# Optimization experiments

Hardware: AMD Instinct MI355X
Metric: run time of the kernel (lower is better)

Reference implementation:

```python
import jax, jax.numpy as jnp
import numpy as np

ALPHA = 1.8   # Levy stability index (undefined global in source; chosen heavy-tailed)
BETA = 0.0    # symmetric
SIGMA = 0.5
DEPTH = 25
DIM = 64
HID = 100
BATCH = 262144


def _levy_noise(u_raw, w_raw):
    """Chambers-Mallows-Stuck sampler for symmetric alpha-stable (beta=0).
    u_raw, w_raw ~ U(0,1); returns clipped noise, scale=0.1, clamp [-10,10]."""
    U = jnp.pi * (u_raw - 0.5)                       # U(-pi/2, pi/2)
    W = -jnp.log(jnp.clip(w_raw, 1e-12, 1.0))        # Exp(1)
    inv_a = 1.0 / ALPHA
    X = (jnp.sin(ALPHA * U) / jnp.cos(U) ** inv_a) * \
        (jnp.cos(U - ALPHA * U) / jnp.clip(W, 1e-12, None)) ** ((1.0 - ALPHA) * inv_a)
    return jnp.clip(0.1 * X, -10.0, 10.0)


def setup_inputs() -> dict:
    key = jax.random.key(0)
    ks = jax.random.split(key, 8)
    d, h = DIM, HID
    return {
        "x": jax.random.normal(ks[0], (BATCH, d), dtype=jnp.float32),
        "u_raw": jax.random.uniform(ks[1], (DEPTH, d), dtype=jnp.float32),
        "w_raw": jax.random.uniform(ks[2], (DEPTH, d), dtype=jnp.float32),
        "W_down": jax.random.normal(ks[3], (d, d), dtype=jnp.float32) / np.sqrt(d),
        "b_down": jnp.zeros((d,), jnp.float32),
        "W_drift": jax.random.normal(ks[4], (d, d), dtype=jnp.float32) / np.sqrt(d),
        "b_drift": jnp.zeros((d,), jnp.float32),
        "W1": jax.random.normal(ks[5], (d, h), dtype=jnp.float32) / np.sqrt(d),
        "b1": jnp.zeros((h,), jnp.float32),
        "W2": jax.random.normal(ks[6], (h, 1), dtype=jnp.float32) / np.sqrt(h),
        "b2": jnp.zeros((1,), jnp.float32),
    }


def reference(x, u_raw, w_raw, W_down, b_down, W_drift, b_drift, W1, b1, W2, b2):
    dt = 1.0 / DEPTH
    out = x @ W_down + b_down                                   # [B, d]
    # diffusion logit on the INITIAL state, held fixed through the loop
    logit = jax.nn.relu(out @ W1 + b1) @ W2 + b2                # [B, 1]
    scale = SIGMA * jax.nn.sigmoid(logit) * dt ** (1.0 / ALPHA)  # [B, 1]
    noise = _levy_noise(u_raw, w_raw)                           # [DEPTH, d]

    def step(out, n):
        drift = jax.nn.relu(out @ W_drift + b_drift) + out      # DriftNet: relu(lin)+x
        return out + drift * dt + scale * n, None

    out, _ = jax.lax.scan(step, out, noise)
    drift_out = jax.nn.relu(out @ W_drift + b_drift) + out
    return drift_out, out
```

## Files before the change

### kernel.cpp

```cpp
#include <hip/hip_runtime.h>
#include <hip/hip_bf16.h>

#define DEPTH 25
#define DIM   64
#define HID   100

typedef _Float16 f16x4 __attribute__((ext_vector_type(4)));
typedef float    f32x4 __attribute__((ext_vector_type(4)));
typedef float    f32x2 __attribute__((ext_vector_type(2)));

__global__ __launch_bounds__(64) void levy_noise_kernel(
    const float* __restrict__ u_raw, const float* __restrict__ w_raw,
    float* __restrict__ noise)
{
    const int idx = blockIdx.x * 64 + threadIdx.x;
    if (idx >= DEPTH * DIM) return;
    float u = u_raw[idx];
    float w = w_raw[idx];
    float U  = 3.14159265358979323846f * (u - 0.5f);
    float Wv = -logf(fminf(fmaxf(w, 1e-12f), 1.0f));
    float t1 = sinf(1.8f * U) / powf(cosf(U), 0.5555555555555556f);
    float ratio = cosf(0.8f * U) / fmaxf(Wv, 1e-12f);
    float X = t1 * powf(ratio, -0.4444444444444444f);
    noise[idx] = fminf(fmaxf(0.1f * X, -10.0f), 10.0f);
}

__global__ __launch_bounds__(256) void sdenet_fused(
    const float* __restrict__ x,      const float* __restrict__ noise_g,
    const float* __restrict__ W_down, const float* __restrict__ b_down,
    const float* __restrict__ W_drift,const float* __restrict__ b_drift,
    const float* __restrict__ W1,     const float* __restrict__ b1,
    const float* __restrict__ W2,     const float* __restrict__ b2,
    float* __restrict__ out, int batch)
{
    __shared__ float noise_lds[DEPTH * DIM];

    const int tid = threadIdx.x;
    {
        const float4* src = (const float4*)noise_g;
        float4* dst = (float4*)noise_lds;
        for (int idx = tid; idx < DEPTH * DIM / 4; idx += 256)
            dst[idx] = src[idx];
    }
    __syncthreads();

    const int wave = tid >> 6;
    const int lane = tid & 63;
    const int r    = lane & 15;
    const int g    = lane >> 4;
    const int row  = blockIdx.x * 64 + wave * 16 + r;
    const float dt = 0.04f;

    f16x4 bfrag[4];
    #pragma unroll
    for (int kt = 0; kt < 4; ++kt) {
        const float4 xv = *(const float4*)(x + row * DIM + kt * 16 + g * 4);
        f16x4 t;
        t[0] = (_Float16)xv.x; t[1] = (_Float16)xv.y;
        t[2] = (_Float16)xv.z; t[3] = (_Float16)xv.w;
        bfrag[kt] = t;
    }

    f32x2 out2[4][2];
    #pragma unroll
    for (int Mt = 0; Mt < 4; ++Mt) {
        f32x4 acc = *(const f32x4*)(b_down + Mt * 16 + g * 4);
        #pragma unroll
        for (int kt = 0; kt < 4; ++kt) {
            f16x4 a;
            #pragma unroll
            for (int i = 0; i < 4; ++i)
                a[i] = (_Float16)W_down[(kt * 16 + g * 4 + i) * DIM + Mt * 16 + r];
            acc = __builtin_amdgcn_mfma_f32_16x16x16f16(a, bfrag[kt], acc, 0, 0, 0);
        }
        out2[Mt][0][0] = acc[0]; out2[Mt][0][1] = acc[1];
        out2[Mt][1][0] = acc[2]; out2[Mt][1][1] = acc[3];
    }

    #pragma unroll
    for (int kt = 0; kt < 4; ++kt) {
        f16x4 t;
        t[0] = (_Float16)out2[kt][0][0]; t[1] = (_Float16)out2[kt][0][1];
        t[2] = (_Float16)out2[kt][1][0]; t[3] = (_Float16)out2[kt][1][1];
        bfrag[kt] = t;
    }

    float partial = 0.0f;
    #pragma unroll
    for (int Mt = 0; Mt < 7; ++Mt) {
        f32x4 acc;
        #pragma unroll
        for (int reg = 0; reg < 4; ++reg) {
            int n = Mt * 16 + g * 4 + reg;
            acc[reg] = (n < HID) ? b1[n] : 0.0f;
        }
        const int ncol = Mt * 16 + r;
        #pragma unroll
        for (int kt = 0; kt < 4; ++kt) {
            f16x4 a;
            #pragma unroll
            for (int i = 0; i < 4; ++i) {
                int k = kt * 16 + g * 4 + i;
                float v = (ncol < HID) ? W1[k * HID + ncol] : 0.0f;
                a[i] = (_Float16)v;
            }
            acc = __builtin_amdgcn_mfma_f32_16x16x16f16(a, bfrag[kt], acc, 0, 0, 0);
        }
        #pragma unroll
        for (int reg = 0; reg < 4; ++reg) {
            int n = Mt * 16 + g * 4 + reg;
            if (n < HID) partial += fmaxf(acc[reg], 0.0f) * W2[n];
        }
    }
    partial += __shfl_xor(partial, 16);
    partial += __shfl_xor(partial, 32);
    const float logit = partial + b2[0];
    const float scale = 0.5f * (1.0f / (1.0f + expf(-logit)))
                      * powf(0.04f, 1.0f / 1.8f);
    const f32x2 scale2 = { scale, scale };
    const f32x2 c104   = { 1.04f, 1.04f };
    const f32x2 zero2  = { 0.0f, 0.0f };

    f16x4 aWd[4][4];
    #pragma unroll
    for (int Mt = 0; Mt < 4; ++Mt)
        #pragma unroll
        for (int kt = 0; kt < 4; ++kt) {
            f16x4 a;
            #pragma unroll
            for (int i = 0; i < 4; ++i)
                a[i] = (_Float16)(dt * W_drift[(kt * 16 + g * 4 + i) * DIM + Mt * 16 + r]);
            aWd[Mt][kt] = a;
        }
    f32x4 biasd[4];
    #pragma unroll
    for (int Mt = 0; Mt < 4; ++Mt) {
        f32x4 b = *(const f32x4*)(b_drift + Mt * 16 + g * 4);
        biasd[Mt][0] = b[0] * dt; biasd[Mt][1] = b[1] * dt;
        biasd[Mt][2] = b[2] * dt; biasd[Mt][3] = b[3] * dt;
    }

    for (int t = 0; t < DEPTH; ++t) {
        f32x4 nz[4];
        #pragma unroll
        for (int Mt = 0; Mt < 4; ++Mt)
            nz[Mt] = *(const f32x4*)(noise_lds + t * DIM + Mt * 16 + g * 4);

        f32x4 acc[4];
        #pragma unroll
        for (int Mt = 0; Mt < 4; ++Mt) {
            acc[Mt] = biasd[Mt];
            #pragma unroll
            for (int kt = 0; kt < 4; ++kt)
                acc[Mt] = __builtin_amdgcn_mfma_f32_16x16x16f16(aWd[Mt][kt], bfrag[kt], acc[Mt], 0, 0, 0);
        }
        #pragma unroll
        for (int Mt = 0; Mt < 4; ++Mt) {
            #pragma unroll
            for (int h = 0; h < 2; ++h) {
                f32x2 a2 = { acc[Mt][2 * h], acc[Mt][2 * h + 1] };
                f32x2 n2 = { nz[Mt][2 * h],  nz[Mt][2 * h + 1] };
                f32x2 rel = __builtin_elementwise_max(a2, zero2);
                f32x2 tmp = __builtin_elementwise_fma(out2[Mt][h], c104, rel);
                out2[Mt][h] = __builtin_elementwise_fma(scale2, n2, tmp);
            }
        }
        #pragma unroll
        for (int kt = 0; kt < 4; ++kt) {
            f16x4 tt;
            tt[0] = (_Float16)out2[kt][0][0]; tt[1] = (_Float16)out2[kt][0][1];
            tt[2] = (_Float16)out2[kt][1][0]; tt[3] = (_Float16)out2[kt][1][1];
            bfrag[kt] = tt;
        }
    }

    const long long out2_off = (long long)batch * DIM;
    #pragma unroll
    for (int Mt = 0; Mt < 4; ++Mt) {
        f32x4 acc = biasd[Mt];
        #pragma unroll
        for (int kt = 0; kt < 4; ++kt)
            acc = __builtin_amdgcn_mfma_f32_16x16x16f16(aWd[Mt][kt], bfrag[kt], acc, 0, 0, 0);
        float o0 = out2[Mt][0][0], o1 = out2[Mt][0][1];
        float o2 = out2[Mt][1][0], o3 = out2[Mt][1][1];
        float4 dv, ov;
        dv.x = fmaf(fmaxf(acc[0], 0.0f), 25.0f, o0);
        dv.y = fmaf(fmaxf(acc[1], 0.0f), 25.0f, o1);
        dv.z = fmaf(fmaxf(acc[2], 0.0f), 25.0f, o2);
        dv.w = fmaf(fmaxf(acc[3], 0.0f), 25.0f, o3);
        ov.x = o0; ov.y = o1; ov.z = o2; ov.w = o3;
        *(float4*)(out + (long long)row * DIM + Mt * 16 + g * 4) = dv;
        *(float4*)(out + out2_off + (long long)row * DIM + Mt * 16 + g * 4) = ov;
    }
}

extern "C" void kernel_launch(void* const* d_in, const int* in_sizes, int n_in,
                              void* d_out, int out_size, void* d_ws, size_t ws_size,
                              hipStream_t stream) {
    const float* x       = (const float*)d_in[0];
    const float* u_raw   = (const float*)d_in[1];
    const float* w_raw   = (const float*)d_in[2];
    const float* W_down  = (const float*)d_in[3];
    const float* b_down  = (const float*)d_in[4];
    const float* W_drift = (const float*)d_in[5];
    const float* b_drift = (const float*)d_in[6];
    const float* W1      = (const float*)d_in[7];
    const float* b1      = (const float*)d_in[8];
    const float* W2      = (const float*)d_in[9];
    const float* b2      = (const float*)d_in[10];
    float* out   = (float*)d_out;
    float* noise = (float*)d_ws;

    const int batch = in_sizes[0] / DIM;
    const int blocks = batch / 64;

    levy_noise_kernel<<<DEPTH, 64, 0, stream>>>(u_raw, w_raw, noise);
    sdenet_fused<<<blocks, 256, 0, stream>>>(
        x, noise, W_down, b_down, W_drift, b_drift,
        W1, b1, W2, b2, out, batch);
}
```

Before: 281.0 us.

## Use 16x16x32 f16 MFMA and stage transposed f16 weights in LDS

```diff
diff --git a/kernel.cpp b/kernel.cpp
--- a/kernel.cpp
+++ b/kernel.cpp
@@ -1,11 +1,12 @@
 #include <hip/hip_runtime.h>
-#include <hip/hip_bf16.h>
 
 #define DEPTH 25
 #define DIM   64
 #define HID   100
 
 typedef _Float16 f16x4 __attribute__((ext_vector_type(4)));
+typedef _Float16 f16x8 __attribute__((ext_vector_type(8)));
+typedef __fp16   h2    __attribute__((ext_vector_type(2)));
 typedef float    f32x4 __attribute__((ext_vector_type(4)));
 typedef float    f32x2 __attribute__((ext_vector_type(2)));
 
@@ -25,6 +26,15 @@
     noise[idx] = fminf(fmaxf(0.1f * X, -10.0f), 10.0f);
 }
 
+static __device__ __forceinline__ f16x8 lda8(const _Float16* p) {
+    f16x4 lo = *(const f16x4*)p;
+    f16x4 hi = *(const f16x4*)(p + 16);
+    f16x8 v;
+    v[0] = lo[0]; v[1] = lo[1]; v[2] = lo[2]; v[3] = lo[3];
+    v[4] = hi[0]; v[5] = hi[1]; v[6] = hi[2]; v[7] = hi[3];
+    return v;
+}
+
 __global__ __launch_bounds__(256) void sdenet_fused(
     const float* __restrict__ x,      const float* __restrict__ noise_g,
     const float* __restrict__ W_down, const float* __restrict__ b_down,
@@ -33,17 +43,10 @@
     const float* __restrict__ W2,     const float* __restrict__ b2,
     float* __restrict__ out, int batch)
 {
-    __shared__ float noise_lds[DEPTH * DIM];
-
-    const int tid = threadIdx.x;
-    {
-        const float4* src = (const float4*)noise_g;
-        float4* dst = (float4*)noise_lds;
-        for (int idx = tid; idx < DEPTH * DIM / 4; idx += 256)
-            dst[idx] = src[idx];
-    }
-    __syncthreads();
-
+    __shared__ float    noise_lds[DEPTH * DIM];
+    __shared__ _Float16 wbuf[8192];
+
+    const int tid  = threadIdx.x;
     const int wave = tid >> 6;
     const int lane = tid & 63;
     const int r    = lane & 15;
@@ -51,13 +54,38 @@
     const int row  = blockIdx.x * 64 + wave * 16 + r;
     const float dt = 0.04f;
 
-    f16x4 bfrag[4];
-    #pragma unroll
-    for (int kt = 0; kt < 4; ++kt) {
-        const float4 xv = *(const float4*)(x + row * DIM + kt * 16 + g * 4);
-        f16x4 t;
-        t[0] = (_Float16)xv.x; t[1] = (_Float16)xv.y;
-        t[2] = (_Float16)xv.z; t[3] = (_Float16)xv.w;
+    {
+        const float4* src = (const float4*)noise_g;
+        float4* dst = (float4*)noise_lds;
+        for (int idx = tid; idx < DEPTH * DIM / 4; idx += 256)
+            dst[idx] = src[idx];
+    }
+    for (int idx = tid; idx < 2048; idx += 256) {
+        const int m = idx >> 5;
+        const int k = (idx & 31) * 2;
+        *(h2*)(wbuf + m * 64 + k) =
+            __builtin_amdgcn_cvt_pkrtz(W_down[k * DIM + m], W_down[(k + 1) * DIM + m]);
+        *(h2*)(wbuf + 4096 + m * 64 + k) =
+            __builtin_amdgcn_cvt_pkrtz(dt * W_drift[k * DIM + m],
+                                       dt * W_drift[(k + 1) * DIM + m]);
+    }
+
+    float4 xlo[2], xhi[2];
+    #pragma unroll
+    for (int kt = 0; kt < 2; ++kt) {
+        xlo[kt] = *(const float4*)(x + row * DIM + kt * 32 + g * 4);
+        xhi[kt] = *(const float4*)(x + row * DIM + kt * 32 + 16 + g * 4);
+    }
+    __syncthreads();
+
+    f16x8 bfrag[2];
+    #pragma unroll
+    for (int kt = 0; kt < 2; ++kt) {
+        f16x8 t;
+        t[0] = (_Float16)xlo[kt].x; t[1] = (_Float16)xlo[kt].y;
+        t[2] = (_Float16)xlo[kt].z; t[3] = (_Float16)xlo[kt].w;
+        t[4] = (_Float16)xhi[kt].x; t[5] = (_Float16)xhi[kt].y;
+        t[6] = (_Float16)xhi[kt].z; t[7] = (_Float16)xhi[kt].w;
         bfrag[kt] = t;
     }
 
@@ -66,24 +94,52 @@
     for (int Mt = 0; Mt < 4; ++Mt) {
         f32x4 acc = *(const f32x4*)(b_down + Mt * 16 + g * 4);
         #pragma unroll
-        for (int kt = 0; kt < 4; ++kt) {
-            f16x4 a;
-            #pragma unroll
-            for (int i = 0; i < 4; ++i)
-                a[i] = (_Float16)W_down[(kt * 16 + g * 4 + i) * DIM + Mt * 16 + r];
-            acc = __builtin_amdgcn_mfma_f32_16x16x16f16(a, bfrag[kt], acc, 0, 0, 0);
-        }
+        for (int kt = 0; kt < 2; ++kt)
+            acc = __builtin_amdgcn_mfma_f32_16x16x32_f16(
+                lda8(wbuf + (Mt * 16 + r) * 64 + kt * 32 + g * 4),
+                bfrag[kt], acc, 0, 0, 0);
         out2[Mt][0][0] = acc[0]; out2[Mt][0][1] = acc[1];
         out2[Mt][1][0] = acc[2]; out2[Mt][1][1] = acc[3];
     }
 
-    #pragma unroll
-    for (int kt = 0; kt < 4; ++kt) {
-        f16x4 t;
-        t[0] = (_Float16)out2[kt][0][0]; t[1] = (_Float16)out2[kt][0][1];
-        t[2] = (_Float16)out2[kt][1][0]; t[3] = (_Float16)out2[kt][1][1];
-        bfrag[kt] = t;
-    }
+    auto refresh = [&]() {
+        #pragma unroll
+        for (int kt = 0; kt < 2; ++kt) {
+            f16x8 t;
+            t[0] = (_Float16)out2[2*kt  ][0][0]; t[1] = (_Float16)out2[2*kt  ][0][1];
+            t[2] = (_Float16)out2[2*kt  ][1][0]; t[3] = (_Float16)out2[2*kt  ][1][1];
+            t[4] = (_Float16)out2[2*kt+1][0][0]; t[5] = (_Float16)out2[2*kt+1][0][1];
+            t[6] = (_Float16)out2[2*kt+1][1][0]; t[7] = (_Float16)out2[2*kt+1][1][1];
+            bfrag[kt] = t;
+        }
+    };
+    refresh();
+
+    f16x8 aWd[4][2];
+    #pragma unroll
+    for (int Mt = 0; Mt < 4; ++Mt)
+        #pragma unroll
+        for (int kt = 0; kt < 2; ++kt)
+            aWd[Mt][kt] = lda8(wbuf + 4096 + (Mt * 16 + r) * 64 + kt * 32 + g * 4);
+
+    f32x4 biasd[4];
+    #pragma unroll
+    for (int Mt = 0; Mt < 4; ++Mt) {
+        f32x4 b = *(const f32x4*)(b_drift + Mt * 16 + g * 4);
+        biasd[Mt][0] = b[0] * dt; biasd[Mt][1] = b[1] * dt;
+        biasd[Mt][2] = b[2] * dt; biasd[Mt][3] = b[3] * dt;
+    }
+
+    __syncthreads();
+
+    for (int idx = tid; idx < 3584; idx += 256) {
+        const int n = idx >> 5;
+        const int k = (idx & 31) * 2;
+        const float v0 = (n < HID) ? W1[k * HID + n] : 0.0f;
+        const float v1 = (n < HID) ? W1[(k + 1) * HID + n] : 0.0f;
+        *(h2*)(wbuf + n * 64 + k) = __builtin_amdgcn_cvt_pkrtz(v0, v1);
+    }
+    __syncthreads();
 
     float partial = 0.0f;
     #pragma unroll
@@ -91,24 +147,17 @@
         f32x4 acc;
         #pragma unroll
         for (int reg = 0; reg < 4; ++reg) {
-            int n = Mt * 16 + g * 4 + reg;
+            const int n = Mt * 16 + g * 4 + reg;
             acc[reg] = (n < HID) ? b1[n] : 0.0f;
         }
         const int ncol = Mt * 16 + r;
         #pragma unroll
-        for (int kt = 0; kt < 4; ++kt) {
-            f16x4 a;
-            #pragma unroll
-            for (int i = 0; i < 4; ++i) {
-                int k = kt * 16 + g * 4 + i;
-                float v = (ncol < HID) ? W1[k * HID + ncol] : 0.0f;
-                a[i] = (_Float16)v;
-            }
-            acc = __builtin_amdgcn_mfma_f32_16x16x16f16(a, bfrag[kt], acc, 0, 0, 0);
-        }
+        for (int kt = 0; kt < 2; ++kt)
+            acc = __builtin_amdgcn_mfma_f32_16x16x32_f16(
+                lda8(wbuf + ncol * 64 + kt * 32 + g * 4), bfrag[kt], acc, 0, 0, 0);
         #pragma unroll
         for (int reg = 0; reg < 4; ++reg) {
-            int n = Mt * 16 + g * 4 + reg;
+            const int n = Mt * 16 + g * 4 + reg;
             if (n < HID) partial += fmaxf(acc[reg], 0.0f) * W2[n];
         }
     }
@@ -121,25 +170,6 @@
     const f32x2 c104   = { 1.04f, 1.04f };
     const f32x2 zero2  = { 0.0f, 0.0f };
 
-    f16x4 aWd[4][4];
-    #pragma unroll
-    for (int Mt = 0; Mt < 4; ++Mt)
-        #pragma unroll
-        for (int kt = 0; kt < 4; ++kt) {
-            f16x4 a;
-            #pragma unroll
-            for (int i = 0; i < 4; ++i)
-                a[i] = (_Float16)(dt * W_drift[(kt * 16 + g * 4 + i) * DIM + Mt * 16 + r]);
-            aWd[Mt][kt] = a;
-        }
-    f32x4 biasd[4];
-    #pragma unroll
-    for (int Mt = 0; Mt < 4; ++Mt) {
-        f32x4 b = *(const f32x4*)(b_drift + Mt * 16 + g * 4);
-        biasd[Mt][0] = b[0] * dt; biasd[Mt][1] = b[1] * dt;
-        biasd[Mt][2] = b[2] * dt; biasd[Mt][3] = b[3] * dt;
-    }
-
     for (int t = 0; t < DEPTH; ++t) {
         f32x4 nz[4];
         #pragma unroll
@@ -149,38 +179,32 @@
         f32x4 acc[4];
         #pragma unroll
         for (int Mt = 0; Mt < 4; ++Mt) {
-            acc[Mt] = biasd[Mt];
-            #pragma unroll
-            for (int kt = 0; kt < 4; ++kt)
-                acc[Mt] = __builtin_amdgcn_mfma_f32_16x16x16f16(aWd[Mt][kt], bfrag[kt], acc[Mt], 0, 0, 0);
+            acc[Mt] = __builtin_amdgcn_mfma_f32_16x16x32_f16(
+                aWd[Mt][0], bfrag[0], biasd[Mt], 0, 0, 0);
+            acc[Mt] = __builtin_amdgcn_mfma_f32_16x16x32_f16(
+                aWd[Mt][1], bfrag[1], acc[Mt], 0, 0, 0);
         }
         #pragma unroll
         for (int Mt = 0; Mt < 4; ++Mt) {
             #pragma unroll
             for (int h = 0; h < 2; ++h) {
-                f32x2 a2 = { acc[Mt][2 * h], acc[Mt][2 * h + 1] };
-                f32x2 n2 = { nz[Mt][2 * h],  nz[Mt][2 * h + 1] };
+                f32x2 a2 = { acc[Mt][2*h], acc[Mt][2*h+1] };
+                f32x2 n2 = { nz[Mt][2*h],  nz[Mt][2*h+1] };
                 f32x2 rel = __builtin_elementwise_max(a2, zero2);
                 f32x2 tmp = __builtin_elementwise_fma(out2[Mt][h], c104, rel);
                 out2[Mt][h] = __builtin_elementwise_fma(scale2, n2, tmp);
             }
         }
-        #pragma unroll
-        for (int kt = 0; kt < 4; ++kt) {
-            f16x4 tt;
-            tt[0] = (_Float16)out2[kt][0][0]; tt[1] = (_Float16)out2[kt][0][1];
-            tt[2] = (_Float16)out2[kt][1][0]; tt[3] = (_Float16)out2[kt][1][1];
-            bfrag[kt] = tt;
-        }
+        refresh();
     }
 
     const long long out2_off = (long long)batch * DIM;
     #pragma unroll
     for (int Mt = 0; Mt < 4; ++Mt) {
-        f32x4 acc = biasd[Mt];
-        #pragma unroll
-        for (int kt = 0; kt < 4; ++kt)
-            acc = __builtin_amdgcn_mfma_f32_16x16x16f16(aWd[Mt][kt], bfrag[kt], acc, 0, 0, 0);
+        f32x4 acc = __builtin_amdgcn_mfma_f32_16x16x32_f16(
+            aWd[Mt][0], bfrag[0], biasd[Mt], 0, 0, 0);
+        acc = __builtin_amdgcn_mfma_f32_16x16x32_f16(
+            aWd[Mt][1], bfrag[1], acc, 0, 0, 0);
         float o0 = out2[Mt][0][0], o1 = out2[Mt][0][1];
         float o2 = out2[Mt][1][0], o3 = out2[Mt][1][1];
         float4 dv, ov;
```

After: 375.6 us. 33.6% more time.
